# Kernel tuning notes

Measured on AMD Instinct MI355X. Metric: run time of the kernel, lower is better.

## Reference

```python
import jax, jax.numpy as jnp
import numpy as np

# dims matching init_kwargs
L, D, NH = 4, 1024, 16          # num_blocks, embed_dim, num_heads
HD = D // NH                     # head dim
CUR, MEM, BS, IN = 512, 512, 8, 512
FF = 4 * D
GRU_BIAS = 2.0

def sinusoidal_pe(full_seq, dim):
    # SinusoidalPE: freqs = arange(0, dim, 2); inv = 10000**(-freqs/dim); seq descending
    freqs = jnp.arange(0, dim, 2.0)
    inv = 10000.0 ** (-freqs / dim)
    seq = jnp.arange(full_seq - 1, -1, -1.0)
    ang = seq[:, None] * inv[None, :]                       # (full, dim/2)
    return jnp.concatenate([jnp.sin(ang), jnp.cos(ang)], axis=-1)  # (full, dim)

def layer_norm(x, g, b, eps=1e-5):
    m = x.mean(-1, keepdims=True)
    v = ((x - m) ** 2).mean(-1, keepdims=True)
    return (x - m) * jax.lax.rsqrt(v + eps) * g + b

def rel_shift(x):
    # Transformer-XL relative shift. x: (q, k, b, h)
    q, k, b, h = x.shape
    zp = jnp.zeros((q, 1, b, h), x.dtype)
    return jnp.concatenate([zp, x], axis=1).reshape(k + 1, q, b, h)[1:].reshape(q, k, b, h)

def gru_gate(x, y, W):
    # W: (6, D, D) = Wr, Ur, Wz, Uz, Wg, Ug (no bias except learned-ish gru_bias on z)
    Wr, Ur, Wz, Uz, Wg, Ug = W[0], W[1], W[2], W[3], W[4], W[5]
    r = jax.nn.sigmoid(y @ Wr.T + x @ Ur.T)
    z = jax.nn.sigmoid(y @ Wz.T + x @ Uz.T - GRU_BIAS)
    hh = jnp.tanh(y @ Wg.T + (r * x) @ Ug.T)
    return (1.0 - z) * x + z * hh

def rel_attn(q, k, v, pos, U, V, mask, W):
    # q: (cur, bs, D); k, v: (full, bs, D); pos: (full, D); W: (5, D, D) = Wq,Wk,Wv,Wr,Wo
    cur, bs, _ = q.shape
    full = k.shape[0]
    qh = (q @ W[0].T).reshape(cur, bs, NH, HD)
    kh = (k @ W[1].T).reshape(full, bs, NH, HD)
    vh = (v @ W[2].T).reshape(full, bs, NH, HD)
    rh = (pos @ W[3].T).reshape(full, NH, HD)
    AC = jnp.einsum('ibhd,jbhd->ijbh', qh + U, kh)          # content stream with U bias
    BD = rel_shift(jnp.einsum('ibhd,jhd->ijbh', qh + V, rh))  # position stream with V bias
    score = (AC + BD) * (1.0 / np.sqrt(HD))
    score = jnp.where(mask[:, :, None, None], jnp.asarray(-1e30, score.dtype), score)
    attn = jax.nn.softmax(score, axis=1)
    out = jnp.einsum('ijbh,jbhd->ibhd', attn, vh).reshape(cur, bs, D)
    return out @ W[4].T

def gelu(x):
    return jax.nn.gelu(x, approximate=False)  # torch nn.GELU default is exact

def _forward(h, memory, W_emb, b_emb, U, V, ln1, ln2, Wattn, g1, g2, fc_W1, fc_b1, fc_W2, fc_b2):
    h = jnp.transpose(h, (1, 0, 2))            # (cur, bs, in)
    mem = jax.lax.stop_gradient(memory)        # memory holds detached hidden states
    cur = h.shape[0]
    prev = mem.shape[1]
    full = cur + prev
    x = gelu(h @ W_emb.T + b_emb)              # linear embedding + GELU activation
    pos = sinusoidal_pe(full, D)               # (full, D); pos_emb.unsqueeze(1) broadcast over bs
    mask = jnp.triu(jnp.ones((cur, full), bool), 1 + prev)
    out = x
    for i in range(L):
        key = jnp.concatenate([mem[i], out], axis=0)   # (full, bs, D)
        nq = layer_norm(out, ln1[i, 0], ln1[i, 1])
        nk = layer_norm(key, ln1[i, 0], ln1[i, 1])
        Y = rel_attn(nq, nk, nk, pos, U, V, mask, Wattn[i])
        Y = gelu(Y)                                     # dropout is identity (eval / p=0)
        o1 = gru_gate(out, Y, g1[i])
        E = layer_norm(o1, ln2[i, 0], ln2[i, 1])
        E = gelu(gelu(E @ fc_W1[i].T + fc_b1[i]) @ fc_W2[i].T + fc_b2[i])
        out = gru_gate(o1, E, g2[i])
    return jnp.transpose(out, (1, 0, 2))       # (bs, cur, D)

def setup_inputs() -> dict:
    key = jax.random.key(0)
    ks = jax.random.split(key, 12)
    s = 0.02
    eye2 = jnp.stack([jnp.ones(D, jnp.float32), jnp.zeros(D, jnp.float32)])  # (gamma, beta)
    return {
        'h': jax.random.normal(ks[0], (BS, CUR, IN), jnp.float32),
        'memory': jax.random.normal(ks[1], (L, MEM, BS, D), jnp.float32),
        'W_emb': jax.random.normal(ks[2], (D, IN), jnp.float32) * s,
        'b_emb': jnp.zeros((D,), jnp.float32),
        'U': jax.random.normal(ks[3], (NH, HD), jnp.float32) * s,
        'V': jax.random.normal(ks[4], (NH, HD), jnp.float32) * s,
        'ln1': jnp.tile(eye2[None], (L, 1, 1)),
        'ln2': jnp.tile(eye2[None], (L, 1, 1)),
        'Wattn': jax.random.normal(ks[5], (L, 5, D, D), jnp.float32) * s,  # q,k,v,r,o per block
        'g1': jax.random.normal(ks[6], (L, 6, D, D), jnp.float32) * s,
        'g2': jax.random.normal(ks[7], (L, 6, D, D), jnp.float32) * s,
        'fc_W1': jax.random.normal(ks[8], (L, FF, D), jnp.float32) * s,
        'fc_b1': jnp.zeros((L, FF), jnp.float32),
        'fc_W2': jax.random.normal(ks[9], (L, D, FF), jnp.float32) * s,
        'fc_b2': jnp.zeros((L, D), jnp.float32),
    }

def reference(h, memory, W_emb, b_emb, U, V, ln1, ln2, Wattn, g1, g2, fc_W1, fc_b1, fc_W2, fc_b2):
    return _forward(h, memory, W_emb, b_emb, U, V, ln1, ln2, Wattn, g1, g2, fc_W1, fc_b1, fc_W2, fc_b2)
```

## Files before the change

kernel.cpp:

```cpp
#include <hip/hip_runtime.h>
#include <hip/hip_bf16.h>


typedef __attribute__((ext_vector_type(8))) __bf16 bfrag;
typedef __attribute__((ext_vector_type(4))) float f4;
typedef __attribute__((ext_vector_type(4))) unsigned short u16x4;
typedef __attribute__((ext_vector_type(8))) unsigned short u16x8;

__device__ __forceinline__ unsigned short f2bf(float f){
  union { float f; unsigned u; } v; v.f = f;
  unsigned r = v.u + 0x7fffu + ((v.u >> 16) & 1u);
  return (unsigned short)(r >> 16);
}
__device__ __forceinline__ float bf2f(unsigned short u){
  union { unsigned u; float f; } v; v.u = (unsigned)u << 16; return v.f;
}
__device__ __forceinline__ float geluf(float x){
  return 0.5f * x * (1.0f + erff(x * 0.7071067811865476f));
}
__device__ __forceinline__ float sigm(float x){ return 1.0f/(1.0f + __expf(-x)); }

__device__ __forceinline__ void gl_lds(const void* g, void* l){
  __builtin_amdgcn_global_load_lds(
    reinterpret_cast<const __attribute__((address_space(1))) unsigned int*>(
        reinterpret_cast<unsigned long>(g)),
    reinterpret_cast<__attribute__((address_space(3))) unsigned int*>(
        reinterpret_cast<unsigned long>(l)),
    16, 0, 0);
}

struct GP {
  const unsigned short* A;
  const unsigned short* A2;
  const unsigned short* B;
  const unsigned short* B2;
  unsigned short* O1;
  unsigned short* O2;
  unsigned short* O3;
  unsigned short* O4;
  unsigned short* O5;
  float* OF;
  const float* bias1;
  const float* bias2;
  const float* X;
  const float* Z;
  int K, Ksplit, lda, ldb, ldo;
  int sBz;
};

template<int BM, int BN, int EPI>
__global__ __launch_bounds__(256) void gemm_k(GP p){
  __shared__ unsigned short As[2][BM*32];
  __shared__ unsigned short Bs[2][BN*32];
  const int tid  = threadIdx.x;
  const int lane = tid & 63;
  const int wid  = tid >> 6;
  const int lr   = lane & 15;
  const int lg   = lane >> 4;
  constexpr int FM = BM/32, FN = BN/32;
  const int m0 = blockIdx.y * BM;
  const int n0 = blockIdx.x * BN;
  const int z  = blockIdx.z;

  const unsigned short* Abase = p.A;
  const unsigned short* Bbase = p.B;
  if constexpr (EPI==13){
    if (z==2){ if (blockIdx.y >= 32) return; Abase = p.A + 4194304; }
    if (z==3){ if (blockIdx.y >= 8)  return; Abase = p.A2; }
    const int zsel = (z==0)?1:((z==1)?2:((z==2)?0:3));
    Bbase = p.B + (long)zsel*1048576;
  }

  const int ksp = p.Ksplit ? p.Ksplit : p.K;
  const unsigned short* AbL = Abase + (long)m0*p.lda;
  const unsigned short* AbH = p.A2 && EPI!=13 ? (p.A2 + (long)m0*p.lda - ksp) : AbL;
  const unsigned short* BbL = Bbase + (long)z*p.sBz + (long)n0*p.ldb;
  const unsigned short* BbH = p.B2 ? (p.B2 + (long)z*p.sBz + (long)n0*p.ldb - ksp) : BbL;

  const int srow = tid >> 2;
  const int skk  = (tid & 3) * 8;

  f4 acc[FM][FN];
  f4 zero4 = {0.0f, 0.0f, 0.0f, 0.0f};
  #pragma unroll
  for (int m=0;m<FM;m++)
    #pragma unroll
    for (int n=0;n<FN;n++) acc[m][n] = zero4;

  const int nk = p.K >> 5;
  #pragma unroll
  for (int q=0;q<BM/64;q++)
    gl_lds(AbL + (long)(q*64 + srow)*p.lda + skk, (char*)As[0] + q*4096 + wid*1024);
  #pragma unroll
  for (int q=0;q<BN/64;q++)
    gl_lds(BbL + (long)(q*64 + srow)*p.ldb + skk, (char*)Bs[0] + q*4096 + wid*1024);
  __syncthreads();

  int cur = 0;
  for (int t = 0; t < nk; ++t){
    const int k1 = (t+1) << 5;
    if (t+1 < nk){
      const unsigned short* A_ = (k1 < ksp) ? AbL : AbH;
      const unsigned short* B_ = (k1 < ksp) ? BbL : BbH;
      #pragma unroll
      for (int q=0;q<BM/64;q++)
        gl_lds(A_ + (long)(q*64 + srow)*p.lda + k1 + skk, (char*)As[cur^1] + q*4096 + wid*1024);
      #pragma unroll
      for (int q=0;q<BN/64;q++)
        gl_lds(B_ + (long)(q*64 + srow)*p.ldb + k1 + skk, (char*)Bs[cur^1] + q*4096 + wid*1024);
    }
    bfrag af[FM], bfr[FN];
    #pragma unroll
    for (int m=0;m<FM;m++)
      af[m] = *(const bfrag*)&As[cur][((wid>>1)*(BM/2) + m*16 + lr)*32 + lg*8];
    #pragma unroll
    for (int n=0;n<FN;n++)
      bfr[n] = *(const bfrag*)&Bs[cur][((wid&1)*(BN/2) + n*16 + lr)*32 + lg*8];
    #pragma unroll
    for (int m=0;m<FM;m++)
      #pragma unroll
      for (int n=0;n<FN;n++)
        acc[m][n] = __builtin_amdgcn_mfma_f32_16x16x32_bf16(af[m], bfr[n], acc[m][n], 0, 0, 0);
    __syncthreads();
    cur ^= 1;
  }

  const int wr0 = m0 + (wid>>1)*(BM/2);
  const int wc0 = n0 + (wid&1)*(BN/2);
  #pragma unroll
  for (int m=0;m<FM;m++)
    #pragma unroll
    for (int n=0;n<FN;n++)
      #pragma unroll
      for (int r=0;r<4;r++){
        const int gr = wr0 + m*16 + lg*4 + r;
        const int gc = wc0 + n*16 + lr;
        const float a = acc[m][n][r];
        const long base = (long)gr*p.ldo + gc;
        if constexpr (EPI==6){
          const float t = a + (p.bias1 ? p.bias1[gc] : 0.0f);
          p.O1[base] = f2bf(geluf(t));
        }
        else if constexpr (EPI==7){
          const float t = geluf(a + p.bias1[gc]);
          p.OF[base] = t; p.O1[base] = f2bf(t);
        }
        else if constexpr (EPI==11){
          const long ix = (long)gr*1024 + gc;
          if (z==0) p.O1[ix] = f2bf(sigm(a) * p.X[ix]);
          else      p.OF[ix] = sigm(a - 2.0f);
        }
        else if constexpr (EPI==12){
          const long ix = (long)gr*1024 + gc;
          const float zz = p.Z[ix];
          const float oo = (1.0f - zz)*p.X[ix] + zz*tanhf(a);
          p.OF[ix] = oo; p.O1[ix] = f2bf(oo);
        }
        else if constexpr (EPI==13){
          const long ix = (long)gr*1024 + gc;
          if (z==0){ p.O1[ix] = f2bf(a); }
          else if (z==1){
            const int b_ = gr & 7, js = gr >> 3, h_ = gc >> 6, d_ = gc & 63;
            p.O2[(long)(b_*16 + h_)*65536 + (long)d_*1024 + js] = f2bf(a);
          }
          else if (z==2){ p.O3[ix] = f2bf((a + p.bias1[gc])*0.125f);
                          p.O4[ix] = f2bf((a + p.bias2[gc])*0.125f); }
          else { p.O5[ix] = f2bf(a); }
        }
      }
}

__global__ __launch_bounds__(256,3) void attn_k(const unsigned short* __restrict__ qU,
                                                const unsigned short* __restrict__ qV,
                                                const unsigned short* __restrict__ kh,
                                                const unsigned short* __restrict__ rh,
                                                const unsigned short* __restrict__ vhT,
                                                unsigned short* __restrict__ ctx){
  __shared__ char Sm[20480];
  __shared__ float redm[4][16];
  __shared__ float reds[4][16];
  __shared__ float invd[16];
  const int tid = threadIdx.x;
  const int w   = tid >> 6;
  const int lane= tid & 63;
  const int lr  = lane & 15;
  const int lg  = lane >> 4;
  const int id = blockIdx.x;
  const int b  = id & 7;
  const int i0 = ((id >> 3) & 31) * 16;
  const int h  = id >> 8;
  const int gmax = i0 >> 4;
  const long hoff = (long)h * 64;
  const f4 z4 = {0.f,0.f,0.f,0.f};

  bfrag bqv[2];
  #pragma unroll
  for (int kk=0;kk<2;kk++)
    bqv[kk] = *(const bfrag*)(qV + ((long)(i0 + lr)*8 + b)*1024 + hoff + kk*32 + lg*8);
  bfrag aq[2];
  #pragma unroll
  for (int kk=0;kk<2;kk++)
    aq[kk] = *(const bfrag*)(qU + ((long)(i0 + lr)*8 + b)*1024 + hoff + kk*32 + lg*8);

  f4 s[16];
  #pragma unroll
  for (int n=0;n<16;n++) s[n] = (f4){-1e30f,-1e30f,-1e30f,-1e30f};

  #pragma unroll
  for (int half=0; half<2; ++half){
    const int c0    = half*512;
    const int rbase = half ? (1008 - i0) : (496 - i0);
    const int ntil  = half ? (gmax + 1) : 33;
    const int radd  = half ? -497 : 15;
    for (int mt = w; mt < ntil; mt += 4){
      const int r0 = rbase + mt*16;
      f4 acc = z4;
      #pragma unroll
      for (int kk=0;kk<2;kk++){
        bfrag ar = *(const bfrag*)(rh + (long)(r0 + lr)*1024 + hoff + kk*32 + lg*8);
        acc = __builtin_amdgcn_mfma_f32_16x16x32_bf16(ar, bqv[kk], acc, 0,0,0);
      }
      #pragma unroll
      for (int q=0;q<4;q++){
        const int rr = mt*16 + lg*4 + q;
        *(unsigned short*)(Sm + rr*38 + lr*2) = f2bf(acc[q]);
      }
    }
    __syncthreads();
    #pragma unroll
    for (int n=0;n<8;n++){
      const int g = 2*w + ((n>>1)<<3) + (n&1);
      if (half==1 && g > gmax) continue;
      const int cb = c0 + w*32 + (n>>1)*128 + (n&1)*16;
      f4 a = z4;
      #pragma unroll
      for (int kk=0;kk<2;kk++){
        bfrag bk = *(const bfrag*)(kh + ((long)(cb + lr)*8 + b)*1024 + hoff + kk*32 + lg*8);
        a = __builtin_amdgcn_mfma_f32_16x16x32_bf16(aq[kk], bk, a, 0,0,0);
      }
      #pragma unroll
      for (int q=0;q<4;q++){
        const int di = lg*4 + q;
        const int jc = cb + lr;
        if (jc > i0 + di + 512) a[q] = -1e30f;
        else {
          const int rr = jc - di + radd;
          a[q] += bf2f(*(const unsigned short*)(Sm + rr*38 + di*2));
        }
      }
      s[half*8 + n] = a;
    }
    __syncthreads();
  }

  float mx[4], sum[4];
  #pragma unroll
  for (int q=0;q<4;q++){
    float m = s[0][q];
    #pragma unroll
    for (int n=1;n<16;n++) m = fmaxf(m, s[n][q]);
    m = fmaxf(m, __shfl_xor(m, 1));
    m = fmaxf(m, __shfl_xor(m, 2));
    m = fmaxf(m, __shfl_xor(m, 4));
    m = fmaxf(m, __shfl_xor(m, 8));
    if (lr == 0) redm[w][lg*4+q] = m;
  }
  __syncthreads();
  #pragma unroll
  for (int q=0;q<4;q++){
    const int row = lg*4+q;
    mx[q] = fmaxf(fmaxf(redm[0][row], redm[1][row]), fmaxf(redm[2][row], redm[3][row]));
    sum[q] = 0.0f;
  }
  #pragma unroll
  for (int n=0;n<16;n++)
    #pragma unroll
    for (int q=0;q<4;q++){
      const float e = __expf(s[n][q] - mx[q]);
      s[n][q] = e;
      sum[q] += e;
    }
  #pragma unroll
  for (int q=0;q<4;q++){
    float v = sum[q];
    v += __shfl_xor(v, 1);
    v += __shfl_xor(v, 2);
    v += __shfl_xor(v, 4);
    v += __shfl_xor(v, 8);
    if (lr == 0) reds[w][lg*4+q] = v;
  }
  __syncthreads();
  if (tid < 16)
    invd[tid] = 1.0f / (reds[0][tid] + reds[1][tid] + reds[2][tid] + reds[3][tid]);

  f4 oac[4];
  #pragma unroll
  for (int nd=0;nd<4;nd++) oac[nd] = z4;
  const unsigned short* vb_base = vhT + (long)(b*16 + h)*65536;
  char* Pch = Sm + w*1024;
  #pragma unroll
  for (int t=0;t<8;t++){
    const int hh_ = t>>2, tt = t&3;
    if (hh_==1 && (2*w + 8*tt) > gmax) continue;
    const int jb = hh_*512 + w*32 + tt*128;
    #pragma unroll
    for (int nn=0;nn<2;nn++){
      const f4 e = s[hh_*8 + tt*2 + nn];
      #pragma unroll
      for (int q=0;q<4;q++){
        const int row = lg*4 + q;
        const int col = nn*16 + lr;
        *(unsigned short*)(Pch + row*64 + ((col*2) ^ (((row>>2)&3)<<4))) = f2bf(e[q]);
      }
    }
    bfrag pa = *(const bfrag*)(Pch + lr*64 + ((lg*16) ^ (((lr>>2)&3)<<4)));
    #pragma unroll
    for (int nd=0;nd<4;nd++){
      bfrag bv = *(const bfrag*)(vb_base + (long)(nd*16 + lr)*1024 + jb + lg*8);
      oac[nd] = __builtin_amdgcn_mfma_f32_16x16x32_bf16(pa, bv, oac[nd], 0,0,0);
    }
  }
  float* po = (float*)(Sm + 4096 + w*4096);
  #pragma unroll
  for (int nd=0;nd<4;nd++)
    #pragma unroll
    for (int q=0;q<4;q++)
      po[(lg*4+q)*64 + nd*16 + lr] = oac[nd][q];
  __syncthreads();
  {
    const int row = tid >> 4;
    const int d0  = (tid & 15) * 4;
    f4 v = *(const f4*)(Sm + 4096 + (row*64 + d0)*4);
    #pragma unroll
    for (int ww=1;ww<4;ww++){
      const f4 u = *(const f4*)(Sm + 4096 + ww*4096 + (row*64 + d0)*4);
      v.x += u.x; v.y += u.y; v.z += u.z; v.w += u.w;
    }
    const float iv = invd[row];
    u16x4 o;
    o.x = f2bf(v.x*iv); o.y = f2bf(v.y*iv); o.z = f2bf(v.z*iv); o.w = f2bf(v.w*iv);
    *(u16x4*)(ctx + ((long)(i0 + row)*8 + b)*1024 + hoff + d0) = o;
  }
}

__global__ __launch_bounds__(256) void ln_k(const float* __restrict__ srcA,
                                            const float* __restrict__ srcB, int splitRow,
                                            const float* __restrict__ g, const float* __restrict__ b,
                                            unsigned short* __restrict__ dst){
  const int row = blockIdx.x;
  const float* src = (srcB != nullptr && row >= splitRow)
                       ? (srcB + (long)(row - splitRow)*1024)
                       : (srcA + (long)row*1024);
  const int t = threadIdx.x;
  float4 v = ((const float4*)src)[t];
  float s1 = v.x+v.y+v.z+v.w;
  float s2 = v.x*v.x+v.y*v.y+v.z*v.z+v.w*v.w;
  #pragma unroll
  for (int o=32;o;o>>=1){ s1 += __shfl_xor(s1,o); s2 += __shfl_xor(s2,o); }
  __shared__ float r1[4], r2[4];
  const int w = t>>6;
  if ((t&63)==0){ r1[w]=s1; r2[w]=s2; }
  __syncthreads();
  s1 = r1[0]+r1[1]+r1[2]+r1[3];
  s2 = r2[0]+r2[1]+r2[2]+r2[3];
  const float mean = s1*(1.0f/1024.0f);
  const float var  = s2*(1.0f/1024.0f) - mean*mean;
  const float rs   = rsqrtf(var + 1e-5f);
  float4 gg = ((const float4*)g)[t];
  float4 bb = ((const float4*)b)[t];
  u16x4 o;
  o.x = f2bf((v.x-mean)*rs*gg.x + bb.x);
  o.y = f2bf((v.y-mean)*rs*gg.y + bb.y);
  o.z = f2bf((v.z-mean)*rs*gg.z + bb.z);
  o.w = f2bf((v.w-mean)*rs*gg.w + bb.w);
  *(u16x4*)(dst + (long)row*1024 + t*4) = o;
}

__global__ __launch_bounds__(256) void conv_k(const float* __restrict__ s,
                                              unsigned short* __restrict__ d, long n){
  long i = ((long)blockIdx.x*256 + threadIdx.x)*4;
  if (i >= n) return;
  float4 v = *(const float4*)(s + i);
  u16x4 o; o.x=f2bf(v.x); o.y=f2bf(v.y); o.z=f2bf(v.z); o.w=f2bf(v.w);
  *(u16x4*)(d + i) = o;
}

__global__ __launch_bounds__(128) void ht_k(const float* __restrict__ h,
                                            unsigned short* __restrict__ d){
  const int row = blockIdx.x;
  const int i = row>>3, b = row&7;
  const float* src = h + ((long)b*512 + i)*512;
  const int t = threadIdx.x;
  float4 v = ((const float4*)src)[t];
  u16x4 o; o.x=f2bf(v.x); o.y=f2bf(v.y); o.z=f2bf(v.z); o.w=f2bf(v.w);
  *(u16x4*)(d + (long)row*512 + t*4) = o;
}

__global__ __launch_bounds__(256) void pos_k(unsigned short* __restrict__ d){
  const int r = blockIdx.x, t = threadIdx.x;
  const float seq = (float)(1023 - r);
  u16x4 o;
  #pragma unroll
  for (int q=0;q<4;q++){
    const int c = t*4 + q;
    const int f = (c < 512) ? c : (c - 512);
    const float inv = expf((float)f * -0.017988946039016f);
    const float ang = seq * inv;
    const float val = (c < 512) ? sinf(ang) : cosf(ang);
    o[q] = f2bf(val);
  }
  *(u16x4*)(d + (long)r*1024 + t*4) = o;
}

__global__ __launch_bounds__(256) void outT_k(const float* __restrict__ o,
                                              float* __restrict__ d){
  const int row = blockIdx.x;
  const int b = row>>9, i = row&511;
  const float4 v = ((const float4*)(o + ((long)i*8 + b)*1024))[threadIdx.x];
  ((float4*)(d + (long)row*1024))[threadIdx.x] = v;
}

extern "C" void kernel_launch(void* const* d_in, const int* in_sizes, int n_in,
                              void* d_out, int out_size, void* d_ws, size_t ws_size,
                              hipStream_t stream){
  (void)in_sizes; (void)n_in; (void)out_size; (void)ws_size;
  const float* h     = (const float*)d_in[0];
  const float* memin = (const float*)d_in[1];
  const float* Wemb  = (const float*)d_in[2];
  const float* bemb  = (const float*)d_in[3];
  const float* Ub    = (const float*)d_in[4];
  const float* Vb    = (const float*)d_in[5];
  const float* ln1   = (const float*)d_in[6];
  const float* ln2   = (const float*)d_in[7];
  const float* Wattn = (const float*)d_in[8];
  const float* g1w   = (const float*)d_in[9];
  const float* g2w   = (const float*)d_in[10];
  const float* fw1   = (const float*)d_in[11];
  const float* fb1   = (const float*)d_in[12];
  const float* fw2   = (const float*)d_in[13];
  const float* fb2   = (const float*)d_in[14];

  char* Wp = (char*)d_ws;
  size_t off = 0;
  auto take = [&](size_t bytes)->size_t{ size_t r = off; off += (bytes + 255) & ~(size_t)255; return r; };
  float*          outf = (float*)         (Wp + take(16777216));
  unsigned short* xbf  = (unsigned short*)(Wp + take( 8388608));
  float*          o1f  = (float*)         (Wp + take(16777216));
  unsigned short* o1b  = (unsigned short*)(Wp + take( 8388608));
  float*          zbf  = (float*)         (Wp + take(16777216));
  unsigned short* rxb  = (unsigned short*)(Wp + take( 8388608));
  unsigned short* yb   = (unsigned short*)(Wp + take( 8388608));
  unsigned short* Eb   = (unsigned short*)(Wp + take( 8388608));
  unsigned short* wb0  = (unsigned short*)(Wp + take(52428800));
  unsigned short* hTb  = (unsigned short*)(Wp + take( 4194304));
  unsigned short* webb = (unsigned short*)(Wp + take( 1048576));
  unsigned short* posb = (unsigned short*)(Wp + take( 2097152));
  unsigned short* nkb  = (unsigned short*)(Wp + take(16777216));
  unsigned short* qUb  = (unsigned short*)(Wp + take( 8388608));
  unsigned short* qVb  = (unsigned short*)(Wp + take( 8388608));
  unsigned short* khb  = (unsigned short*)(Wp + take(16777216));
  unsigned short* vhTb = (unsigned short*)(Wp + take(16777216));
  unsigned short* F1b  = khb;
  unsigned short* rhb  = (unsigned short*)(Wp + take( 2097152));
  unsigned short* ctxb = (unsigned short*)(Wp + take( 8388608));

  const int M1 = 1048576;

  conv_k<<<512, 256, 0, stream>>>(Wemb, webb, 524288);
  ht_k<<<4096, 128, 0, stream>>>(h, hTb);
  pos_k<<<1024, 256, 0, stream>>>(posb);

  {
    GP p{}; p.A=hTb; p.B=webb; p.OF=outf; p.O1=xbf; p.bias1=bemb;
    p.K=512; p.lda=512; p.ldb=512; p.ldo=1024;
    gemm_k<128,64,7><<<dim3(16,32,1),256,0,stream>>>(p);
  }

  auto gru_fn = [&](const unsigned short* xb, const float* xf, const unsigned short* yb_,
                    const unsigned short* w6, float* of, unsigned short* ob){
    { GP p{}; p.A=yb_; p.A2=xb; p.B=w6; p.B2=w6+M1; p.sBz=2*M1;
      p.O1=rxb; p.OF=zbf; p.X=xf;
      p.K=2048; p.Ksplit=1024; p.lda=1024; p.ldb=1024; p.ldo=1024;
      gemm_k<128,128,11><<<dim3(8,32,2),256,0,stream>>>(p); }
    { GP p{}; p.A=yb_; p.A2=rxb; p.B=w6+4*M1; p.B2=w6+5*M1;
      p.X=xf; p.Z=zbf; p.OF=of; p.O1=ob;
      p.K=2048; p.Ksplit=1024; p.lda=1024; p.ldb=1024; p.ldo=1024;
      gemm_k<128,64,12><<<dim3(16,32,1),256,0,stream>>>(p); }
  };

  for (int l = 0; l < 4; ++l){
    conv_k<<<5120,256,0,stream>>>(Wattn + (long)l*5242880, wb0,          5242880);
    conv_k<<<6144,256,0,stream>>>(g1w   + (long)l*6291456, wb0 +  5*M1,  6291456);
    conv_k<<<6144,256,0,stream>>>(g2w   + (long)l*6291456, wb0 + 11*M1,  6291456);
    conv_k<<<4096,256,0,stream>>>(fw1   + (long)l*4194304, wb0 + 17*M1,  4194304);
    conv_k<<<4096,256,0,stream>>>(fw2   + (long)l*4194304, wb0 + 21*M1,  4194304);

    ln_k<<<8192,256,0,stream>>>(memin + (long)l*4194304, outf, 4096,
                                ln1 + l*2048, ln1 + l*2048 + 1024, nkb);

    {
      GP p{}; p.A=nkb; p.A2=posb; p.B=wb0;
      p.O1=khb; p.O2=vhTb; p.O3=qUb; p.O4=qVb; p.O5=rhb;
      p.bias1=Ub; p.bias2=Vb;
      p.K=1024; p.lda=1024; p.ldb=1024; p.ldo=1024;
      gemm_k<128,128,13><<<dim3(8,64,4),256,0,stream>>>(p); }

    attn_k<<<4096,256,0,stream>>>(qUb, qVb, khb, rhb, vhTb, ctxb);

    {
      GP p{}; p.A=ctxb; p.B=wb0+4*M1; p.O1=yb;
      p.K=1024; p.lda=1024; p.ldb=1024; p.ldo=1024;
      gemm_k<128,64,6><<<dim3(16,32,1),256,0,stream>>>(p); }

    gru_fn(xbf, outf, yb, wb0 + 5*M1, o1f, o1b);

    ln_k<<<4096,256,0,stream>>>(o1f, nullptr, 1<<30,
                                ln2 + l*2048, ln2 + l*2048 + 1024, Eb);

    { GP p{}; p.A=Eb;  p.B=wb0+17*M1; p.O1=F1b; p.bias1=fb1 + l*4096;
      p.K=1024; p.lda=1024; p.ldb=1024; p.ldo=4096;
      gemm_k<128,128,6><<<dim3(32,32,1),256,0,stream>>>(p); }
    { GP p{}; p.A=F1b; p.B=wb0+21*M1; p.O1=yb; p.bias1=fb2 + l*1024;
      p.K=4096; p.lda=4096; p.ldb=4096; p.ldo=1024;
      gemm_k<128,64,6><<<dim3(16,32,1),256,0,stream>>>(p); }

    gru_fn(o1b, o1f, yb, wb0 + 11*M1, outf, xbf);
  }

  outT_k<<<4096,256,0,stream>>>(outf, (float*)d_out);
}
```

Baseline: 2.753 ms.

## Deepen GEMM K-stage, prefetch attention operands, shrink GEMM tiles, raise attn occupancy

The GEMM main loop now stages 64 K-elements per barrier as two 32-wide sub-tiles, which halves the number of synchronisations at the cost of double the shared memory. The attention kernel software-pipelines its global loads of rh, kh and vhT fragments into registers one step ahead of the MFMAs, and its launch bounds ask for 4 blocks per CU instead of 3. Several GEMM launches switch from 128x128 to 128x64 tiles to get more blocks in flight. The added register prefetch buffers may conflict with the higher occupancy target and cause spilling.

```diff
diff --git a/kernel.cpp b/kernel.cpp
--- a/kernel.cpp
+++ b/kernel.cpp
@@ -50,8 +50,8 @@
 
 template<int BM, int BN, int EPI>
 __global__ __launch_bounds__(256) void gemm_k(GP p){
-  __shared__ unsigned short As[2][BM*32];
-  __shared__ unsigned short Bs[2][BN*32];
+  __shared__ unsigned short As[2][2][BM*32];
+  __shared__ unsigned short Bs[2][2][BN*32];
   const int tid  = threadIdx.x;
   const int lane = tid & 63;
   const int wid  = tid >> 6;
@@ -87,40 +87,42 @@
     #pragma unroll
     for (int n=0;n<FN;n++) acc[m][n] = zero4;
 
-  const int nk = p.K >> 5;
-  #pragma unroll
-  for (int q=0;q<BM/64;q++)
-    gl_lds(AbL + (long)(q*64 + srow)*p.lda + skk, (char*)As[0] + q*4096 + wid*1024);
-  #pragma unroll
-  for (int q=0;q<BN/64;q++)
-    gl_lds(BbL + (long)(q*64 + srow)*p.ldb + skk, (char*)Bs[0] + q*4096 + wid*1024);
+  auto stage = [&](int buf, int sub, int k0){
+    const unsigned short* A_ = (k0 < ksp) ? AbL : AbH;
+    #pragma unroll
+    for (int q=0;q<BM/64;q++)
+      gl_lds(A_ + (long)(q*64 + srow)*p.lda + k0 + skk, (char*)As[buf][sub] + q*4096 + wid*1024);
+    const unsigned short* B_ = (k0 < ksp) ? BbL : BbH;
+    #pragma unroll
+    for (int q=0;q<BN/64;q++)
+      gl_lds(B_ + (long)(q*64 + srow)*p.ldb + k0 + skk, (char*)Bs[buf][sub] + q*4096 + wid*1024);
+  };
+
+  const int nk2 = p.K >> 6;
+  stage(0,0,0); stage(0,1,32);
   __syncthreads();
 
   int cur = 0;
-  for (int t = 0; t < nk; ++t){
-    const int k1 = (t+1) << 5;
-    if (t+1 < nk){
-      const unsigned short* A_ = (k1 < ksp) ? AbL : AbH;
-      const unsigned short* B_ = (k1 < ksp) ? BbL : BbH;
-      #pragma unroll
-      for (int q=0;q<BM/64;q++)
-        gl_lds(A_ + (long)(q*64 + srow)*p.lda + k1 + skk, (char*)As[cur^1] + q*4096 + wid*1024);
-      #pragma unroll
-      for (int q=0;q<BN/64;q++)
-        gl_lds(B_ + (long)(q*64 + srow)*p.ldb + k1 + skk, (char*)Bs[cur^1] + q*4096 + wid*1024);
-    }
-    bfrag af[FM], bfr[FN];
-    #pragma unroll
-    for (int m=0;m<FM;m++)
-      af[m] = *(const bfrag*)&As[cur][((wid>>1)*(BM/2) + m*16 + lr)*32 + lg*8];
-    #pragma unroll
-    for (int n=0;n<FN;n++)
-      bfr[n] = *(const bfrag*)&Bs[cur][((wid&1)*(BN/2) + n*16 + lr)*32 + lg*8];
-    #pragma unroll
-    for (int m=0;m<FM;m++)
+  for (int t = 0; t < nk2; ++t){
+    if (t+1 < nk2){
+      stage(cur^1, 0, (t+1)*64);
+      stage(cur^1, 1, (t+1)*64 + 32);
+    }
+    #pragma unroll
+    for (int sub=0; sub<2; ++sub){
+      bfrag af[FM], bfr[FN];
+      #pragma unroll
+      for (int m=0;m<FM;m++)
+        af[m] = *(const bfrag*)&As[cur][sub][((wid>>1)*(BM/2) + m*16 + lr)*32 + lg*8];
       #pragma unroll
       for (int n=0;n<FN;n++)
-        acc[m][n] = __builtin_amdgcn_mfma_f32_16x16x32_bf16(af[m], bfr[n], acc[m][n], 0, 0, 0);
+        bfr[n] = *(const bfrag*)&Bs[cur][sub][((wid&1)*(BN/2) + n*16 + lr)*32 + lg*8];
+      #pragma unroll
+      for (int m=0;m<FM;m++)
+        #pragma unroll
+        for (int n=0;n<FN;n++)
+          acc[m][n] = __builtin_amdgcn_mfma_f32_16x16x32_bf16(af[m], bfr[n], acc[m][n], 0, 0, 0);
+    }
     __syncthreads();
     cur ^= 1;
   }
@@ -170,7 +172,7 @@
       }
 }
 
-__global__ __launch_bounds__(256,3) void attn_k(const unsigned short* __restrict__ qU,
+__global__ __launch_bounds__(256,4) void attn_k(const unsigned short* __restrict__ qU,
                                                 const unsigned short* __restrict__ qV,
                                                 const unsigned short* __restrict__ kh,
                                                 const unsigned short* __restrict__ rh,
@@ -203,8 +205,6 @@
     aq[kk] = *(const bfrag*)(qU + ((long)(i0 + lr)*8 + b)*1024 + hoff + kk*32 + lg*8);
 
   f4 s[16];
-  #pragma unroll
-  for (int n=0;n<16;n++) s[n] = (f4){-1e30f,-1e30f,-1e30f,-1e30f};
 
   #pragma unroll
   for (int half=0; half<2; ++half){
@@ -212,46 +212,85 @@
     const int rbase = half ? (1008 - i0) : (496 - i0);
     const int ntil  = half ? (gmax + 1) : 33;
     const int radd  = half ? -497 : 15;
-    for (int mt = w; mt < ntil; mt += 4){
-      const int r0 = rbase + mt*16;
-      f4 acc = z4;
-      #pragma unroll
-      for (int kk=0;kk<2;kk++){
-        bfrag ar = *(const bfrag*)(rh + (long)(r0 + lr)*1024 + hoff + kk*32 + lg*8);
-        acc = __builtin_amdgcn_mfma_f32_16x16x32_bf16(ar, bqv[kk], acc, 0,0,0);
+    bfrag ar[2][2];
+    if (w < ntil){
+      #pragma unroll
+      for (int kk=0;kk<2;kk++)
+        ar[0][kk] = *(const bfrag*)(rh + (long)(rbase + w*16 + lr)*1024 + hoff + kk*32 + lg*8);
+    }
+    #pragma unroll
+    for (int it=0; it<9; ++it){
+      const int mt = w + it*4;
+      if (mt < ntil){
+        const int mtn = mt + 4;
+        if (mtn < ntil){
+          #pragma unroll
+          for (int kk=0;kk<2;kk++)
+            ar[(it+1)&1][kk] = *(const bfrag*)(rh + (long)(rbase + mtn*16 + lr)*1024 + hoff + kk*32 + lg*8);
+        }
+        f4 acc = z4;
+        #pragma unroll
+        for (int kk=0;kk<2;kk++)
+          acc = __builtin_amdgcn_mfma_f32_16x16x32_bf16(ar[it&1][kk], bqv[kk], acc, 0,0,0);
+        #pragma unroll
+        for (int q=0;q<4;q++){
+          const int rr = mt*16 + lg*4 + q;
+          *(unsigned short*)(Sm + rr*38 + lr*2) = f2bf(acc[q]);
+        }
       }
-      #pragma unroll
-      for (int q=0;q<4;q++){
-        const int rr = mt*16 + lg*4 + q;
-        *(unsigned short*)(Sm + rr*38 + lr*2) = f2bf(acc[q]);
+    }
+    __syncthreads();
+    int nv = 8;
+    if (half==1){
+      nv = 0;
+      #pragma unroll
+      for (int n=0;n<8;n++)
+        if ((2*w + 8*(n>>1) + (n&1)) <= gmax) nv++;
+    }
+    bfrag bk[2][2];
+    if (nv > 0){
+      const int cb0 = c0 + w*32;
+      #pragma unroll
+      for (int kk=0;kk<2;kk++)
+        bk[0][kk] = *(const bfrag*)(kh + ((long)(cb0 + lr)*8 + b)*1024 + hoff + kk*32 + lg*8);
+    }
+    #pragma unroll
+    for (int n=0;n<8;n++){
+      if (n+1 < nv){
+        const int cbn = c0 + w*32 + ((n+1)>>1)*128 + ((n+1)&1)*16;
+        #pragma unroll
+        for (int kk=0;kk<2;kk++)
+          bk[(n+1)&1][kk] = *(const bfrag*)(kh + ((long)(cbn + lr)*8 + b)*1024 + hoff + kk*32 + lg*8);
       }
+      if (n < nv){
+        const int cb = c0 + w*32 + (n>>1)*128 + (n&1)*16;
+        f4 a = z4;
+        #pragma unroll
+        for (int kk=0;kk<2;kk++)
+          a = __builtin_amdgcn_mfma_f32_16x16x32_bf16(aq[kk], bk[n&1][kk], a, 0,0,0);
+        #pragma unroll
+        for (int q=0;q<4;q++){
+          const int di = lg*4 + q;
+          const int jc = cb + lr;
+          if (jc > i0 + di + 512) a[q] = -1e30f;
+          else {
+            const int rr = jc - di + radd;
+            a[q] += bf2f(*(const unsigned short*)(Sm + rr*38 + di*2));
+          }
+        }
+        s[half*8 + n] = a;
+      } else {
+        s[half*8 + n] = (f4){-1e30f,-1e30f,-1e30f,-1e30f};
+      }
     }
     __syncthreads();
-    #pragma unroll
-    for (int n=0;n<8;n++){
-      const int g = 2*w + ((n>>1)<<3) + (n&1);
-      if (half==1 && g > gmax) continue;
-      const int cb = c0 + w*32 + (n>>1)*128 + (n&1)*16;
-      f4 a = z4;
-      #pragma unroll
-      for (int kk=0;kk<2;kk++){
-        bfrag bk = *(const bfrag*)(kh + ((long)(cb + lr)*8 + b)*1024 + hoff + kk*32 + lg*8);
-        a = __builtin_amdgcn_mfma_f32_16x16x32_bf16(aq[kk], bk, a, 0,0,0);
-      }
-      #pragma unroll
-      for (int q=0;q<4;q++){
-        const int di = lg*4 + q;
-        const int jc = cb + lr;
-        if (jc > i0 + di + 512) a[q] = -1e30f;
-        else {
-          const int rr = jc - di + radd;
-          a[q] += bf2f(*(const unsigned short*)(Sm + rr*38 + di*2));
-        }
-      }
-      s[half*8 + n] = a;
-    }
-    __syncthreads();
-  }
+  }
+
+  const unsigned short* vb_base = vhT + (long)(b*16 + h)*65536;
+  bfrag vb[4];
+  #pragma unroll
+  for (int nd=0;nd<4;nd++)
+    vb[nd] = *(const bfrag*)(vb_base + (long)(nd*16 + lr)*1024 + (w*32) + lg*8);
 
   float mx[4], sum[4];
   #pragma unroll
@@ -296,28 +335,36 @@
   f4 oac[4];
   #pragma unroll
   for (int nd=0;nd<4;nd++) oac[nd] = z4;
-  const unsigned short* vb_base = vhT + (long)(b*16 + h)*65536;
   char* Pch = Sm + w*1024;
   #pragma unroll
   for (int t=0;t<8;t++){
     const int hh_ = t>>2, tt = t&3;
-    if (hh_==1 && (2*w + 8*tt) > gmax) continue;
-    const int jb = hh_*512 + w*32 + tt*128;
-    #pragma unroll
-    for (int nn=0;nn<2;nn++){
-      const f4 e = s[hh_*8 + tt*2 + nn];
-      #pragma unroll
-      for (int q=0;q<4;q++){
-        const int row = lg*4 + q;
-        const int col = nn*16 + lr;
-        *(unsigned short*)(Pch + row*64 + ((col*2) ^ (((row>>2)&3)<<4))) = f2bf(e[q]);
+    const bool val = (hh_==0) || ((2*w + 8*tt) <= gmax);
+    if (val){
+      #pragma unroll
+      for (int nn=0;nn<2;nn++){
+        const f4 e = s[hh_*8 + tt*2 + nn];
+        #pragma unroll
+        for (int q=0;q<4;q++){
+          const int row = lg*4 + q;
+          const int col = nn*16 + lr;
+          *(unsigned short*)(Pch + row*64 + ((col*2) ^ (((row>>2)&3)<<4))) = f2bf(e[q]);
+        }
       }
-    }
-    bfrag pa = *(const bfrag*)(Pch + lr*64 + ((lg*16) ^ (((lr>>2)&3)<<4)));
-    #pragma unroll
-    for (int nd=0;nd<4;nd++){
-      bfrag bv = *(const bfrag*)(vb_base + (long)(nd*16 + lr)*1024 + jb + lg*8);
-      oac[nd] = __builtin_amdgcn_mfma_f32_16x16x32_bf16(pa, bv, oac[nd], 0,0,0);
+      bfrag pa = *(const bfrag*)(Pch + lr*64 + ((lg*16) ^ (((lr>>2)&3)<<4)));
+      #pragma unroll
+      for (int nd=0;nd<4;nd++)
+        oac[nd] = __builtin_amdgcn_mfma_f32_16x16x32_bf16(pa, vb[nd], oac[nd], 0,0,0);
+    }
+    if (t+1 < 8){
+      const int h2 = (t+1)>>2, t2 = (t+1)&3;
+      const bool v2 = (h2==0) || ((2*w + 8*t2) <= gmax);
+      if (v2){
+        const int jb2 = h2*512 + w*32 + t2*128;
+        #pragma unroll
+        for (int nd=0;nd<4;nd++)
+          vb[nd] = *(const bfrag*)(vb_base + (long)(nd*16 + lr)*1024 + jb2 + lg*8);
+      }
     }
   }
   float* po = (float*)(Sm + 4096 + w*4096);
@@ -481,7 +528,7 @@
     { GP p{}; p.A=yb_; p.A2=xb; p.B=w6; p.B2=w6+M1; p.sBz=2*M1;
       p.O1=rxb; p.OF=zbf; p.X=xf;
       p.K=2048; p.Ksplit=1024; p.lda=1024; p.ldb=1024; p.ldo=1024;
-      gemm_k<128,128,11><<<dim3(8,32,2),256,0,stream>>>(p); }
+      gemm_k<128,64,11><<<dim3(16,32,2),256,0,stream>>>(p); }
     { GP p{}; p.A=yb_; p.A2=rxb; p.B=w6+4*M1; p.B2=w6+5*M1;
       p.X=xf; p.Z=zbf; p.OF=of; p.O1=ob;
       p.K=2048; p.Ksplit=1024; p.lda=1024; p.ldb=1024; p.ldo=1024;
@@ -503,7 +550,7 @@
       p.O1=khb; p.O2=vhTb; p.O3=qUb; p.O4=qVb; p.O5=rhb;
       p.bias1=Ub; p.bias2=Vb;
       p.K=1024; p.lda=1024; p.ldb=1024; p.ldo=1024;
-      gemm_k<128,128,13><<<dim3(8,64,4),256,0,stream>>>(p); }
+      gemm_k<128,64,13><<<dim3(16,64,4),256,0,stream>>>(p); }
 
     attn_k<<<4096,256,0,stream>>>(qUb, qVb, khb, rhb, vhTb, ctxb);
 
@@ -519,7 +566,7 @@
 
     { GP p{}; p.A=Eb;  p.B=wb0+17*M1; p.O1=F1b; p.bias1=fb1 + l*4096;
       p.K=1024; p.lda=1024; p.ldb=1024; p.ldo=4096;
-      gemm_k<128,128,6><<<dim3(32,32,1),256,0,stream>>>(p); }
+      gemm_k<128,64,6><<<dim3(64,32,1),256,0,stream>>>(p); }
     { GP p{}; p.A=F1b; p.B=wb0+21*M1; p.O1=yb; p.bias1=fb2 + l*1024;
       p.K=4096; p.lda=4096; p.ldb=4096; p.ldo=1024;
       gemm_k<128,64,6><<<dim3(16,32,1),256,0,stream>>>(p); }
```

Measured after the change: 2.733 ms. Within noise of the previous version (-0.7%).

## Deepen GEMM K-step, swizzle block order, shrink tiles, fuse weight conversions

Applied to the files above, without the earlier changes.

The GEMM kernel now stages two 32-wide K slices per iteration (64 per step), which doubles LDS use and halves the number of barriers. Workgroup IDs are remapped in groups of 8 to change the tile traversal order for cache locality. Several GEMMs move from 128x128 to 128x64 tiles for more workgroups, attention launch bounds are raised to 4 waves per SIMD, and the five per-layer weight conversion launches are merged into one kernel. Together these aim to cut launch overhead and sync cost and to raise occupancy, at the cost of more LDS per block and possible register pressure in attention.

```diff
diff --git a/kernel.cpp b/kernel.cpp
--- a/kernel.cpp
+++ b/kernel.cpp
@@ -50,23 +50,35 @@
 
 template<int BM, int BN, int EPI>
 __global__ __launch_bounds__(256) void gemm_k(GP p){
-  __shared__ unsigned short As[2][BM*32];
-  __shared__ unsigned short Bs[2][BN*32];
+  __shared__ unsigned short As[2][2][BM*32];
+  __shared__ unsigned short Bs[2][2][BN*32];
   const int tid  = threadIdx.x;
   const int lane = tid & 63;
   const int wid  = tid >> 6;
   const int lr   = lane & 15;
   const int lg   = lane >> 4;
   constexpr int FM = BM/32, FN = BN/32;
-  const int m0 = blockIdx.y * BM;
-  const int n0 = blockIdx.x * BN;
+
+  int bx = blockIdx.x, by = blockIdx.y;
+  {
+    const int gx = gridDim.x;
+    const int nwg = gx * gridDim.y;
+    if ((nwg & 7) == 0){
+      const int bid = by*gx + bx;
+      const int vid = (bid & 7)*(nwg >> 3) + (bid >> 3);
+      bx = vid % gx;
+      by = vid / gx;
+    }
+  }
+  const int m0 = by * BM;
+  const int n0 = bx * BN;
   const int z  = blockIdx.z;
 
   const unsigned short* Abase = p.A;
   const unsigned short* Bbase = p.B;
   if constexpr (EPI==13){
-    if (z==2){ if (blockIdx.y >= 32) return; Abase = p.A + 4194304; }
-    if (z==3){ if (blockIdx.y >= 8)  return; Abase = p.A2; }
+    if (z==2){ if (by >= 32) return; Abase = p.A + 4194304; }
+    if (z==3){ if (by >= 8)  return; Abase = p.A2; }
     const int zsel = (z==0)?1:((z==1)?2:((z==2)?0:3));
     Bbase = p.B + (long)zsel*1048576;
   }
@@ -87,40 +99,42 @@
     #pragma unroll
     for (int n=0;n<FN;n++) acc[m][n] = zero4;
 
-  const int nk = p.K >> 5;
-  #pragma unroll
-  for (int q=0;q<BM/64;q++)
-    gl_lds(AbL + (long)(q*64 + srow)*p.lda + skk, (char*)As[0] + q*4096 + wid*1024);
-  #pragma unroll
-  for (int q=0;q<BN/64;q++)
-    gl_lds(BbL + (long)(q*64 + srow)*p.ldb + skk, (char*)Bs[0] + q*4096 + wid*1024);
+  auto stage = [&](int buf, int sub, int k0){
+    const unsigned short* A_ = (k0 < ksp) ? AbL : AbH;
+    #pragma unroll
+    for (int q=0;q<BM/64;q++)
+      gl_lds(A_ + (long)(q*64 + srow)*p.lda + k0 + skk, (char*)As[buf][sub] + q*4096 + wid*1024);
+    const unsigned short* B_ = (k0 < ksp) ? BbL : BbH;
+    #pragma unroll
+    for (int q=0;q<BN/64;q++)
+      gl_lds(B_ + (long)(q*64 + srow)*p.ldb + k0 + skk, (char*)Bs[buf][sub] + q*4096 + wid*1024);
+  };
+
+  const int nk2 = p.K >> 6;
+  stage(0,0,0); stage(0,1,32);
   __syncthreads();
 
   int cur = 0;
-  for (int t = 0; t < nk; ++t){
-    const int k1 = (t+1) << 5;
-    if (t+1 < nk){
-      const unsigned short* A_ = (k1 < ksp) ? AbL : AbH;
-      const unsigned short* B_ = (k1 < ksp) ? BbL : BbH;
-      #pragma unroll
-      for (int q=0;q<BM/64;q++)
-        gl_lds(A_ + (long)(q*64 + srow)*p.lda + k1 + skk, (char*)As[cur^1] + q*4096 + wid*1024);
-      #pragma unroll
-      for (int q=0;q<BN/64;q++)
-        gl_lds(B_ + (long)(q*64 + srow)*p.ldb + k1 + skk, (char*)Bs[cur^1] + q*4096 + wid*1024);
-    }
-    bfrag af[FM], bfr[FN];
-    #pragma unroll
-    for (int m=0;m<FM;m++)
-      af[m] = *(const bfrag*)&As[cur][((wid>>1)*(BM/2) + m*16 + lr)*32 + lg*8];
-    #pragma unroll
-    for (int n=0;n<FN;n++)
-      bfr[n] = *(const bfrag*)&Bs[cur][((wid&1)*(BN/2) + n*16 + lr)*32 + lg*8];
-    #pragma unroll
-    for (int m=0;m<FM;m++)
+  for (int t = 0; t < nk2; ++t){
+    if (t+1 < nk2){
+      stage(cur^1, 0, (t+1)*64);
+      stage(cur^1, 1, (t+1)*64 + 32);
+    }
+    #pragma unroll
+    for (int sub=0; sub<2; ++sub){
+      bfrag af[FM], bfr[FN];
+      #pragma unroll
+      for (int m=0;m<FM;m++)
+        af[m] = *(const bfrag*)&As[cur][sub][((wid>>1)*(BM/2) + m*16 + lr)*32 + lg*8];
       #pragma unroll
       for (int n=0;n<FN;n++)
-        acc[m][n] = __builtin_amdgcn_mfma_f32_16x16x32_bf16(af[m], bfr[n], acc[m][n], 0, 0, 0);
+        bfr[n] = *(const bfrag*)&Bs[cur][sub][((wid&1)*(BN/2) + n*16 + lr)*32 + lg*8];
+      #pragma unroll
+      for (int m=0;m<FM;m++)
+        #pragma unroll
+        for (int n=0;n<FN;n++)
+          acc[m][n] = __builtin_amdgcn_mfma_f32_16x16x32_bf16(af[m], bfr[n], acc[m][n], 0, 0, 0);
+    }
     __syncthreads();
     cur ^= 1;
   }
@@ -170,7 +184,7 @@
       }
 }
 
-__global__ __launch_bounds__(256,3) void attn_k(const unsigned short* __restrict__ qU,
+__global__ __launch_bounds__(256,4) void attn_k(const unsigned short* __restrict__ qU,
                                                 const unsigned short* __restrict__ qV,
                                                 const unsigned short* __restrict__ kh,
                                                 const unsigned short* __restrict__ rh,
@@ -383,6 +397,24 @@
   float4 v = *(const float4*)(s + i);
   u16x4 o; o.x=f2bf(v.x); o.y=f2bf(v.y); o.z=f2bf(v.z); o.w=f2bf(v.w);
   *(u16x4*)(d + i) = o;
+}
+
+__global__ __launch_bounds__(256) void conv5_k(const float* __restrict__ wat,
+                                               const float* __restrict__ g1,
+                                               const float* __restrict__ g2,
+                                               const float* __restrict__ f1,
+                                               const float* __restrict__ f2,
+                                               unsigned short* __restrict__ dst){
+  const long i = ((long)blockIdx.x*256 + threadIdx.x)*4;
+  const float* s; long off;
+  if      (i <  5242880){ s = wat; off = 0; }
+  else if (i < 11534336){ s = g1;  off = 5242880; }
+  else if (i < 17825792){ s = g2;  off = 11534336; }
+  else if (i < 22020096){ s = f1;  off = 17825792; }
+  else                  { s = f2;  off = 22020096; }
+  float4 v = *(const float4*)(s + (i - off));
+  u16x4 o; o.x=f2bf(v.x); o.y=f2bf(v.y); o.z=f2bf(v.z); o.w=f2bf(v.w);
+  *(u16x4*)(dst + i) = o;
 }
 
 __global__ __launch_bounds__(128) void ht_k(const float* __restrict__ h,
@@ -481,7 +513,7 @@
     { GP p{}; p.A=yb_; p.A2=xb; p.B=w6; p.B2=w6+M1; p.sBz=2*M1;
       p.O1=rxb; p.OF=zbf; p.X=xf;
       p.K=2048; p.Ksplit=1024; p.lda=1024; p.ldb=1024; p.ldo=1024;
-      gemm_k<128,128,11><<<dim3(8,32,2),256,0,stream>>>(p); }
+      gemm_k<128,64,11><<<dim3(16,32,2),256,0,stream>>>(p); }
     { GP p{}; p.A=yb_; p.A2=rxb; p.B=w6+4*M1; p.B2=w6+5*M1;
       p.X=xf; p.Z=zbf; p.OF=of; p.O1=ob;
       p.K=2048; p.Ksplit=1024; p.lda=1024; p.ldb=1024; p.ldo=1024;
@@ -489,11 +521,11 @@
   };
 
   for (int l = 0; l < 4; ++l){
-    conv_k<<<5120,256,0,stream>>>(Wattn + (long)l*5242880, wb0,          5242880);
-    conv_k<<<6144,256,0,stream>>>(g1w   + (long)l*6291456, wb0 +  5*M1,  6291456);
-    conv_k<<<6144,256,0,stream>>>(g2w   + (long)l*6291456, wb0 + 11*M1,  6291456);
-    conv_k<<<4096,256,0,stream>>>(fw1   + (long)l*4194304, wb0 + 17*M1,  4194304);
-    conv_k<<<4096,256,0,stream>>>(fw2   + (long)l*4194304, wb0 + 21*M1,  4194304);
+    conv5_k<<<25600,256,0,stream>>>(Wattn + (long)l*5242880,
+                                    g1w   + (long)l*6291456,
+                                    g2w   + (long)l*6291456,
+                                    fw1   + (long)l*4194304,
+                                    fw2   + (long)l*4194304, wb0);
 
     ln_k<<<8192,256,0,stream>>>(memin + (long)l*4194304, outf, 4096,
                                 ln1 + l*2048, ln1 + l*2048 + 1024, nkb);
@@ -503,7 +535,7 @@
       p.O1=khb; p.O2=vhTb; p.O3=qUb; p.O4=qVb; p.O5=rhb;
       p.bias1=Ub; p.bias2=Vb;
       p.K=1024; p.lda=1024; p.ldb=1024; p.ldo=1024;
-      gemm_k<128,128,13><<<dim3(8,64,4),256,0,stream>>>(p); }
+      gemm_k<128,64,13><<<dim3(16,64,4),256,0,stream>>>(p); }
 
     attn_k<<<4096,256,0,stream>>>(qUb, qVb, khb, rhb, vhTb, ctxb);
 
@@ -519,7 +551,7 @@
 
     { GP p{}; p.A=Eb;  p.B=wb0+17*M1; p.O1=F1b; p.bias1=fb1 + l*4096;
       p.K=1024; p.lda=1024; p.ldb=1024; p.ldo=4096;
-      gemm_k<128,128,6><<<dim3(32,32,1),256,0,stream>>>(p); }
+      gemm_k<128,64,6><<<dim3(64,32,1),256,0,stream>>>(p); }
     { GP p{}; p.A=F1b; p.B=wb0+21*M1; p.O1=yb; p.bias1=fb2 + l*1024;
       p.K=4096; p.lda=4096; p.ldb=4096; p.ldo=1024;
       gemm_k<128,64,6><<<dim3(16,32,1),256,0,stream>>>(p); }
```

Measured after the change: 2.687 ms. -2.4%, faster.
